# Performance work log

Measured on AMD Instinct MI355X. Metric: run time of the kernel, lower is better.

## Reference

```python
import jax, jax.numpy as jnp
import numpy as np

KS = 3
N = KS * KS
PAD = 1


def conv2d(x, w, b, stride=1, pad=0):
    out = jax.lax.conv_general_dilated(x, w, (stride, stride), [(pad, pad), (pad, pad)],
                                       dimension_numbers=('NCHW', 'OIHW', 'NCHW'))
    return out + b[None, :, None, None]


def lrelu(x):
    return jnp.where(x > 0, x, 0.2 * x)


# bicubic x2 upsample: half-pixel centers, cubic a=-0.75, replicate edges (matches torch F.interpolate bicubic)
_W_F75 = np.array([-0.03515625, 0.26171875, 0.87890625, -0.10546875], np.float32)  # frac 0.75 (even out idx)
_W_F25 = _W_F75[::-1].copy()  # frac 0.25 (odd out idx)


def _up2_axis(x, axis):
    n = x.shape[axis]
    j = np.arange(2 * n)
    c = (j + 0.5) / 2.0 - 0.5
    i0 = np.floor(c).astype(np.int32)
    taps = np.clip(i0[:, None] + np.arange(-1, 3)[None, :], 0, n - 1)  # [2n,4]
    w = np.where((j % 2 == 0)[:, None], _W_F75[None, :], _W_F25[None, :]).astype(np.float32)
    xm = jnp.moveaxis(x, axis, -1)
    g = xm[..., jnp.asarray(taps)]  # [..., 2n, 4]
    out = jnp.einsum('...jt,jt->...j', g, jnp.asarray(w))
    return jnp.moveaxis(out, -1, axis)


def bicubic_up2(x):
    return _up2_axis(_up2_axis(x, 2), 3)


def head(x, cw, cb, ra_w, ra_b, rb_w, rb_b):
    # Conv5x5 -> LReLU -> ResBlock -> LReLU
    h = lrelu(conv2d(x, cw, cb, pad=2))
    r = conv2d(lrelu(conv2d(h, ra_w, ra_b, pad=1)), rb_w, rb_b, pad=1) + h
    return lrelu(r)


def aligned_forward(x, query, ref, c1_w, c1_b, r1a_w, r1a_b, r1b_w, r1b_b,
                    p1_w, p1_b, r2a_w, r2a_b, r2b_w, r2b_b, p2_w, p2_b):
    q_up = bicubic_up2(query)
    rf = head(ref, c1_w, c1_b, r1a_w, r1a_b, r1b_w, r1b_b)
    qf = head(q_up, c1_w, c1_b, r1a_w, r1a_b, r1b_w, r1b_b)
    cat = jnp.concatenate([rf, qf], axis=1)
    h1 = lrelu(conv2d(cat, p1_w, p1_b, pad=2))
    h1 = lrelu(conv2d(lrelu(conv2d(h1, r2a_w, r2a_b, pad=1)), r2b_w, r2b_b, pad=1) + h1)
    aff = conv2d(h1, p2_w, p2_b, pad=0) + 1.0
    aff = jnp.clip(aff, -3.0, 3.0)
    b, _, h, w = aff.shape
    aff = jnp.transpose(aff, (0, 2, 3, 1))  # [b,h,w,3]
    s_x = aff[..., 0:1]
    s_y = aff[..., 1:2]
    theta = (aff[..., 2:3] - 1.0) * 1.0472
    vals = jnp.array([-1.5, -0.5, 0.5], aff.dtype)  # kernel offsets for ks=3
    pn_x = jnp.repeat(vals, KS)  # [N]
    pn_y = jnp.tile(vals, KS)
    px0 = pn_x * s_x  # [b,h,w,N] scaled kernel offsets
    py0 = pn_y * s_y
    ct = jnp.cos(theta)
    st = jnp.sin(theta)
    rx = px0 * ct - py0 * st  # rotate
    ry = px0 * st + py0 * ct
    px = rx + 1.5 + (jnp.arange(h, dtype=aff.dtype) + 1.0)[None, :, None, None]
    py = ry + 1.5 + (jnp.arange(w, dtype=aff.dtype) + 1.0)[None, None, :, None]
    xp = jnp.pad(x, ((0, 0), (0, 0), (PAD, PAD), (PAD, PAD)), mode='reflect')
    bsz, c, Hp, Wp = xp.shape
    fx = jnp.floor(px)
    fy = jnp.floor(py)
    qltx = jnp.clip(fx, 0, Hp - 1)
    qlty = jnp.clip(fy, 0, Wp - 1)
    qrbx = jnp.clip(fx + 1, 0, Hp - 1)
    qrby = jnp.clip(fy + 1, 0, Wp - 1)
    pxc = jnp.clip(px, 0, Hp - 1)
    pyc = jnp.clip(py, 0, Wp - 1)
    g_lt = (1 + (qltx - pxc)) * (1 + (qlty - pyc))
    g_rb = (1 - (qrbx - pxc)) * (1 - (qrby - pyc))
    g_lb = (1 + (qltx - pxc)) * (1 - (qrby - pyc))
    g_rt = (1 - (qrbx - pxc)) * (1 + (qlty - pyc))
    x_flat = xp.reshape(bsz, c, Hp * Wp)

    def gather(qx, qy):
        idx = (qx.astype(jnp.int32) * Wp + qy.astype(jnp.int32)).reshape(bsz, 1, -1)
        v = jnp.take_along_axis(x_flat, jnp.broadcast_to(idx, (bsz, c, idx.shape[-1])), axis=2)
        return v.reshape(bsz, c, h, w, N)

    align = (g_lt[:, None] * gather(qltx, qlty) + g_rb[:, None] * gather(qrbx, qrby)
             + g_lb[:, None] * gather(qltx, qrby) + g_rt[:, None] * gather(qrbx, qlty))
    # [b,c,h,w,N] -> [b,c,h*ks,w*ks]
    out = align.reshape(bsz, c, h, w, KS, KS).transpose(0, 1, 2, 4, 3, 5).reshape(bsz, c, h * KS, w * KS)
    return out


def setup_inputs() -> dict:
    key = jax.random.key(0)
    ks = jax.random.split(key, 10)

    def W(k, shape):
        fan_in = int(np.prod(shape[1:]))
        return jax.random.normal(k, shape, jnp.float32) / np.sqrt(fan_in)

    return {
        'x': jax.random.normal(ks[0], (2, 32, 256, 256), jnp.float32),
        'query': jax.random.normal(ks[1], (2, 3, 128, 128), jnp.float32),
        'ref': jax.random.normal(ks[2], (2, 3, 256, 256), jnp.float32),
        'c1_w': W(ks[3], (32, 3, 5, 5)), 'c1_b': jnp.zeros((32,), jnp.float32),
        'r1a_w': W(ks[4], (32, 32, 3, 3)), 'r1a_b': jnp.zeros((32,), jnp.float32),
        'r1b_w': W(ks[5], (32, 32, 3, 3)), 'r1b_b': jnp.zeros((32,), jnp.float32),
        'p1_w': W(ks[6], (32, 64, 5, 5)), 'p1_b': jnp.zeros((32,), jnp.float32),
        'r2a_w': W(ks[7], (32, 32, 3, 3)), 'r2a_b': jnp.zeros((32,), jnp.float32),
        'r2b_w': W(ks[8], (32, 32, 3, 3)), 'r2b_b': jnp.zeros((32,), jnp.float32),
        'p2_w': W(ks[9], (3, 32, 1, 1)), 'p2_b': jnp.zeros((3,), jnp.float32),
    }


def reference(x, query, ref, c1_w, c1_b, r1a_w, r1a_b, r1b_w, r1b_b,
              p1_w, p1_b, r2a_w, r2a_b, r2b_w, r2b_b, p2_w, p2_b):
    return aligned_forward(x, query, ref, c1_w, c1_b, r1a_w, r1a_b, r1b_w, r1b_b,
                           p1_w, p1_b, r2a_w, r2a_b, r2b_w, r2b_b, p2_w, p2_b)
```

## Files before the change

### kernel.cpp

```cpp
#include <hip/hip_runtime.h>
#include <math.h>

#define HW 65536

__device__ __forceinline__ float lrelu_f(float v) { return v > 0.f ? v : 0.2f * v; }

__global__ __launch_bounds__(256) void repack_all(
    const float* __restrict__ c1_w, float* __restrict__ wr_c1,
    const float* __restrict__ r1a_w, float* __restrict__ wr_r1a,
    const float* __restrict__ r1b_w, float* __restrict__ wr_r1b,
    const float* __restrict__ p1_w, float* __restrict__ wr_p1,
    const float* __restrict__ r2a_w, float* __restrict__ wr_r2a,
    const float* __restrict__ r2b_w, float* __restrict__ wr_r2b) {
  int i = blockIdx.x * 256 + threadIdx.x;
  const float* src;
  float* dst;
  int IC, KK, base;
  if (i < 2400)        { src = c1_w;  dst = wr_c1;  IC = 3;  KK = 25; base = 0; }
  else if (i < 11616)  { src = r1a_w; dst = wr_r1a; IC = 32; KK = 9;  base = 2400; }
  else if (i < 20832)  { src = r1b_w; dst = wr_r1b; IC = 32; KK = 9;  base = 11616; }
  else if (i < 72032)  { src = p1_w;  dst = wr_p1;  IC = 64; KK = 25; base = 20832; }
  else if (i < 81248)  { src = r2a_w; dst = wr_r2a; IC = 32; KK = 9;  base = 72032; }
  else if (i < 90464)  { src = r2b_w; dst = wr_r2b; IC = 32; KK = 9;  base = 81248; }
  else return;
  int j = i - base;
  int ickk = IC * KK;
  int o = j / ickk;
  int r = j - o * ickk;
  int ic = r / KK;
  int k = r - ic * KK;
  dst[((ic * 4 + (o >> 3)) * KK + k) * 8 + (o & 7)] = src[j];
}

__global__ __launch_bounds__(256) void up2_kernel(const float* __restrict__ q,
                                                  float* __restrict__ out) {
  int gid = blockIdx.x * blockDim.x + threadIdx.x;
  if (gid >= 2 * 3 * HW) return;
  int x = gid & 255;
  int y = (gid >> 8) & 255;
  int pc = gid >> 16;
  const float F[4] = {-0.03515625f, 0.26171875f, 0.87890625f, -0.10546875f};
  int iy[4], ix[4];
  float wy[4], wx[4];
  {
    int k = y >> 1; bool even = !(y & 1); int i0 = even ? k - 1 : k;
#pragma unroll
    for (int t = 0; t < 4; ++t) {
      int ii = i0 - 1 + t;
      iy[t] = min(max(ii, 0), 127);
      wy[t] = even ? F[t] : F[3 - t];
    }
  }
  {
    int k = x >> 1; bool even = !(x & 1); int i0 = even ? k - 1 : k;
#pragma unroll
    for (int t = 0; t < 4; ++t) {
      int ii = i0 - 1 + t;
      ix[t] = min(max(ii, 0), 127);
      wx[t] = even ? F[t] : F[3 - t];
    }
  }
  const float* qp = q + pc * 16384;
  float s = 0.f;
#pragma unroll
  for (int i = 0; i < 4; ++i) {
    float rs = 0.f;
#pragma unroll
    for (int j = 0; j < 4; ++j) rs = fmaf(wx[j], qp[iy[i] * 128 + ix[j]], rs);
    s = fmaf(wy[i], rs, s);
  }
  out[gid] = s;
}


__global__ __launch_bounds__(256) void conv5_c1(const float* __restrict__ in,
                                                const float* __restrict__ wr,
                                                const float* __restrict__ bias,
                                                float* __restrict__ out) {
  __shared__ float sm[3][8][24];
  int blk = blockIdx.x;
  int b = blk >> 10;
  int t = blk & 1023;
  int ty0 = (t >> 4) * 4, tx0 = (t & 15) * 16;
  int tid = threadIdx.x;
  for (int i = tid; i < 3 * 160; i += 256) {
    int ic = i / 160;
    int r2 = i - ic * 160;
    int r = r2 / 20;
    int c = r2 - r * 20;
    int gy = ty0 + r - 2, gx = tx0 + c - 2;
    float v = 0.f;
    if ((unsigned)gy < 256u && (unsigned)gx < 256u) v = in[(b * 3 + ic) * HW + gy * 256 + gx];
    sm[ic][r][c] = v;
  }
  __syncthreads();
  int lane = tid & 63;
  int wv = __builtin_amdgcn_readfirstlane(tid >> 6);
  int py = lane >> 4, px = lane & 15;
  float acc[8];
#pragma unroll
  for (int o = 0; o < 8; ++o) acc[o] = bias[wv * 8 + o];
#pragma unroll
  for (int ic = 0; ic < 3; ++ic) {
    const float* wp = wr + (ic * 4 + wv) * 200;
#pragma unroll
    for (int ky = 0; ky < 5; ++ky)
#pragma unroll
      for (int kx = 0; kx < 5; ++kx) {
        float v = sm[ic][py + ky][px + kx];
        const float* w8 = wp + (ky * 5 + kx) * 8;
#pragma unroll
        for (int o = 0; o < 8; ++o) acc[o] = fmaf(v, w8[o], acc[o]);
      }
  }
  int y = ty0 + py, x = tx0 + px;
#pragma unroll
  for (int o = 0; o < 8; ++o)
    out[(b * 32 + wv * 8 + o) * HW + y * 256 + x] = lrelu_f(acc[o]);
}

template <bool RES>
__global__ __launch_bounds__(256) void conv3_32(const float* __restrict__ in, int in_cs,
                                                const float* __restrict__ wr,
                                                const float* __restrict__ bias,
                                                const float* __restrict__ res,
                                                float* __restrict__ out, int out_cs,
                                                int out_co) {
  __shared__ float sm[32][6][24];
  int blk = blockIdx.x;
  int b = blk >> 10;
  int t = blk & 1023;
  int ty0 = (t >> 4) * 4, tx0 = (t & 15) * 16;
  int tid = threadIdx.x;
  for (int i = tid; i < 32 * 108; i += 256) {
    int ic = i / 108;
    int r2 = i - ic * 108;
    int r = r2 / 18;
    int c = r2 - r * 18;
    int gy = ty0 + r - 1, gx = tx0 + c - 1;
    float v = 0.f;
    if ((unsigned)gy < 256u && (unsigned)gx < 256u)
      v = in[(b * in_cs + ic) * HW + gy * 256 + gx];
    sm[ic][r][c] = v;
  }
  __syncthreads();
  int lane = tid & 63;
  int wv = __builtin_amdgcn_readfirstlane(tid >> 6);
  int py = lane >> 4, px = lane & 15;
  float acc[8];
#pragma unroll
  for (int o = 0; o < 8; ++o) acc[o] = bias[wv * 8 + o];
#pragma unroll 4
  for (int ic = 0; ic < 32; ++ic) {
    const float* wp = wr + (ic * 4 + wv) * 72;
#pragma unroll
    for (int ky = 0; ky < 3; ++ky)
#pragma unroll
      for (int kx = 0; kx < 3; ++kx) {
        float v = sm[ic][py + ky][px + kx];
        const float* w8 = wp + (ky * 3 + kx) * 8;
#pragma unroll
        for (int o = 0; o < 8; ++o) acc[o] = fmaf(v, w8[o], acc[o]);
      }
  }
  int y = ty0 + py, x = tx0 + px;
  int co = out_co + wv * 8;
#pragma unroll
  for (int o = 0; o < 8; ++o) {
    float rv = acc[o];
    if (RES) rv += res[(b * 32 + wv * 8 + o) * HW + y * 256 + x];
    out[(b * out_cs + co + o) * HW + y * 256 + x] = lrelu_f(rv);
  }
}

__global__ __launch_bounds__(256) void conv5_p1(const float* __restrict__ in,
                                                const float* __restrict__ wr,
                                                const float* __restrict__ bias,
                                                float* __restrict__ out) {
  __shared__ float sm[32][8][24];
  int blk = blockIdx.x;
  int b = blk >> 10;
  int t = blk & 1023;
  int ty0 = (t >> 4) * 4, tx0 = (t & 15) * 16;
  int tid = threadIdx.x;
  int lane = tid & 63;
  int wv = __builtin_amdgcn_readfirstlane(tid >> 6);
  int py = lane >> 4, px = lane & 15;
  float acc[8];
#pragma unroll
  for (int o = 0; o < 8; ++o) acc[o] = bias[wv * 8 + o];
#pragma unroll
  for (int ch = 0; ch < 2; ++ch) {
    __syncthreads();
    for (int i = tid; i < 32 * 160; i += 256) {
      int ic = i / 160;
      int r2 = i - ic * 160;
      int r = r2 / 20;
      int c = r2 - r * 20;
      int gy = ty0 + r - 2, gx = tx0 + c - 2;
      float v = 0.f;
      if ((unsigned)gy < 256u && (unsigned)gx < 256u)
        v = in[(b * 64 + ch * 32 + ic) * HW + gy * 256 + gx];
      sm[ic][r][c] = v;
    }
    __syncthreads();
#pragma unroll 2
    for (int ic = 0; ic < 32; ++ic) {
      const float* wp = wr + ((ch * 32 + ic) * 4 + wv) * 200;
#pragma unroll
      for (int ky = 0; ky < 5; ++ky)
#pragma unroll
        for (int kx = 0; kx < 5; ++kx) {
          float v = sm[ic][py + ky][px + kx];
          const float* w8 = wp + (ky * 5 + kx) * 8;
#pragma unroll
          for (int o = 0; o < 8; ++o) acc[o] = fmaf(v, w8[o], acc[o]);
        }
    }
  }
  int y = ty0 + py, x = tx0 + px;
#pragma unroll
  for (int o = 0; o < 8; ++o)
    out[(b * 32 + wv * 8 + o) * HW + y * 256 + x] = lrelu_f(acc[o]);
}

__global__ __launch_bounds__(256) void p2_aff(const float* __restrict__ h2,
                                              const float* __restrict__ w,
                                              const float* __restrict__ bias,
                                              float4* __restrict__ par) {
  int gid = blockIdx.x * 256 + threadIdx.x;
  int b = gid >> 16;
  int p = gid & 65535;
  float a0 = bias[0], a1 = bias[1], a2 = bias[2];
  for (int c = 0; c < 32; ++c) {
    float v = h2[(b * 32 + c) * HW + p];
    a0 = fmaf(v, w[c], a0);
    a1 = fmaf(v, w[32 + c], a1);
    a2 = fmaf(v, w[64 + c], a2);
  }
  a0 = fminf(fmaxf(a0 + 1.f, -3.f), 3.f);
  a1 = fminf(fmaxf(a1 + 1.f, -3.f), 3.f);
  a2 = fminf(fmaxf(a2 + 1.f, -3.f), 3.f);
  float th = (a2 - 1.f) * 1.0472f;
  float4 o;
  o.x = a0;
  o.y = a1;
  o.z = cosf(th);
  o.w = sinf(th);
  par[gid] = o;
}

__device__ __forceinline__ int refl_idx(int k) {
  int s = k - 1;
  s = s < 0 ? -s : s;
  s = s > 255 ? 510 - s : s;
  return s;
}

__global__ __launch_bounds__(256) void sample_kernel(const float* __restrict__ x,
                                                     const float4* __restrict__ par,
                                                     float* __restrict__ out) {
  const int total = 2 * 32 * 768 * 768;
  int stride = gridDim.x * 256;
  for (int gid = blockIdx.x * 256 + threadIdx.x; gid < total; gid += stride) {
    int ox = gid % 768;
    int t1 = gid / 768;
    int oy = t1 % 768;
    int t2 = t1 / 768;
    int c = t2 & 31;
    int b = t2 >> 5;
    int xw = ox / 3;
    int kj = ox - 3 * xw;
    int y = oy / 3;
    int ki = oy - 3 * y;
    float4 pr = par[(b << 16) + y * 256 + xw];
    float px0 = ((float)ki - 1.5f) * pr.x;
    float py0 = ((float)kj - 1.5f) * pr.y;
    float ct = pr.z, st = pr.w;
    float px = px0 * ct - py0 * st + 1.5f + (float)(y + 1);
    float py = px0 * st + py0 * ct + 1.5f + (float)(xw + 1);
    float fx = floorf(px), fy = floorf(py);
    float x0f = fminf(fmaxf(fx, 0.f), 257.f);
    float x1f = fminf(fmaxf(fx + 1.f, 0.f), 257.f);
    float y0f = fminf(fmaxf(fy, 0.f), 257.f);
    float y1f = fminf(fmaxf(fy + 1.f, 0.f), 257.f);
    float pxc = fminf(fmaxf(px, 0.f), 257.f);
    float pyc = fminf(fmaxf(py, 0.f), 257.f);
    float dx0 = 1.f + (x0f - pxc), dx1 = 1.f - (x1f - pxc);
    float dy0 = 1.f + (y0f - pyc), dy1 = 1.f - (y1f - pyc);
    int xi0 = refl_idx((int)x0f), xi1 = refl_idx((int)x1f);
    int yi0 = refl_idx((int)y0f), yi1 = refl_idx((int)y1f);
    const float* xp = x + (size_t)(b * 32 + c) * HW;
    float v = dx0 * dy0 * xp[xi0 * 256 + yi0] + dx1 * dy1 * xp[xi1 * 256 + yi1] +
              dx0 * dy1 * xp[xi0 * 256 + yi1] + dx1 * dy0 * xp[xi1 * 256 + yi0];
    out[gid] = v;
  }
}

extern "C" void kernel_launch(void* const* d_in, const int* in_sizes, int n_in,
                              void* d_out, int out_size, void* d_ws, size_t ws_size,
                              hipStream_t stream) {
  const float* x = (const float*)d_in[0];
  const float* query = (const float*)d_in[1];
  const float* ref = (const float*)d_in[2];
  const float* c1_w = (const float*)d_in[3];
  const float* c1_b = (const float*)d_in[4];
  const float* r1a_w = (const float*)d_in[5];
  const float* r1a_b = (const float*)d_in[6];
  const float* r1b_w = (const float*)d_in[7];
  const float* r1b_b = (const float*)d_in[8];
  const float* p1_w = (const float*)d_in[9];
  const float* p1_b = (const float*)d_in[10];
  const float* r2a_w = (const float*)d_in[11];
  const float* r2a_b = (const float*)d_in[12];
  const float* r2b_w = (const float*)d_in[13];
  const float* r2b_b = (const float*)d_in[14];
  const float* p2_w = (const float*)d_in[15];
  const float* p2_b = (const float*)d_in[16];
  float* out = (float*)d_out;

  float* ws = (float*)d_ws;
  float* qup = ws;
  float* cat = qup + 393216;
  float* t1 = cat + 8388608;
  float* t2 = t1 + 4194304;
  float* h1 = t2 + 4194304;
  float4* par = (float4*)(h1 + 4194304);
  float* wr_c1 = (float*)(par + 131072);
  float* wr_r1a = wr_c1 + 2400;
  float* wr_r1b = wr_r1a + 9216;
  float* wr_p1 = wr_r1b + 9216;
  float* wr_r2a = wr_p1 + 51200;
  float* wr_r2b = wr_r2a + 9216;

  repack_all<<<354, 256, 0, stream>>>(c1_w, wr_c1, r1a_w, wr_r1a, r1b_w, wr_r1b,
                                      p1_w, wr_p1, r2a_w, wr_r2a, r2b_w, wr_r2b);

  up2_kernel<<<1536, 256, 0, stream>>>(query, qup);

  conv5_c1<<<2048, 256, 0, stream>>>(ref, wr_c1, c1_b, t1);
  conv3_32<false><<<2048, 256, 0, stream>>>(t1, 32, wr_r1a, r1a_b, nullptr, t2, 32, 0);
  conv3_32<true><<<2048, 256, 0, stream>>>(t2, 32, wr_r1b, r1b_b, t1, cat, 64, 0);

  conv5_c1<<<2048, 256, 0, stream>>>(qup, wr_c1, c1_b, t1);
  conv3_32<false><<<2048, 256, 0, stream>>>(t1, 32, wr_r1a, r1a_b, nullptr, t2, 32, 0);
  conv3_32<true><<<2048, 256, 0, stream>>>(t2, 32, wr_r1b, r1b_b, t1, cat, 64, 32);

  conv5_p1<<<2048, 256, 0, stream>>>(cat, wr_p1, p1_b, h1);
  conv3_32<false><<<2048, 256, 0, stream>>>(h1, 32, wr_r2a, r2a_b, nullptr, t2, 32, 0);
  conv3_32<true><<<2048, 256, 0, stream>>>(t2, 32, wr_r2b, r2b_b, h1, t1, 32, 0);

  p2_aff<<<512, 256, 0, stream>>>(t1, p2_w, p2_b, par);

  sample_kernel<<<4096, 256, 0, stream>>>(x, par, out);
}
```

Before: 765.4 us.

## Retile convs by output-channel group and hoist sampling coords across channels

The conv kernels now tile 8x32 pixels per block, with one 8-output-channel group per block selected by the block index, and stream input channels through shared memory in chunks of 8. Previously each 4x16 block covered all 32 output channels. This gives every wave the same weights (uniform/scalar loads) and enlarges the spatial tile, cutting halo overhead, but input tiles are now reloaded once per output-channel group. The sampling kernel computes the 9 bilinear offsets and weights once per pixel and reuses them across 8 channels, removing repeated index math. The cost is register pressure and strided, less coalesced output stores (stride 3).

```diff
diff --git a/kernel.cpp b/kernel.cpp
--- a/kernel.cpp
+++ b/kernel.cpp
@@ -77,17 +77,18 @@
                                                 const float* __restrict__ wr,
                                                 const float* __restrict__ bias,
                                                 float* __restrict__ out) {
-  __shared__ float sm[3][8][24];
+  __shared__ float sm[3][12][36];
   int blk = blockIdx.x;
   int b = blk >> 10;
-  int t = blk & 1023;
-  int ty0 = (t >> 4) * 4, tx0 = (t & 15) * 16;
+  int ocg = (blk >> 8) & 3;
+  int tile = blk & 255;
+  int ty0 = (tile >> 3) * 8, tx0 = (tile & 7) * 32;
   int tid = threadIdx.x;
-  for (int i = tid; i < 3 * 160; i += 256) {
-    int ic = i / 160;
-    int r2 = i - ic * 160;
-    int r = r2 / 20;
-    int c = r2 - r * 20;
+  for (int i = tid; i < 3 * 432; i += 256) {
+    int ic = i / 432;
+    int rem = i - ic * 432;
+    int r = rem / 36;
+    int c = rem - r * 36;
     int gy = ty0 + r - 2, gx = tx0 + c - 2;
     float v = 0.f;
     if ((unsigned)gy < 256u && (unsigned)gx < 256u) v = in[(b * 3 + ic) * HW + gy * 256 + gx];
@@ -96,13 +97,13 @@
   __syncthreads();
   int lane = tid & 63;
   int wv = __builtin_amdgcn_readfirstlane(tid >> 6);
-  int py = lane >> 4, px = lane & 15;
+  int py = 2 * wv + (lane >> 5), px = lane & 31;
   float acc[8];
 #pragma unroll
-  for (int o = 0; o < 8; ++o) acc[o] = bias[wv * 8 + o];
+  for (int o = 0; o < 8; ++o) acc[o] = bias[ocg * 8 + o];
 #pragma unroll
   for (int ic = 0; ic < 3; ++ic) {
-    const float* wp = wr + (ic * 4 + wv) * 200;
+    const float* wp = wr + (ic * 4 + ocg) * 200;
 #pragma unroll
     for (int ky = 0; ky < 5; ++ky)
 #pragma unroll
@@ -116,7 +117,7 @@
   int y = ty0 + py, x = tx0 + px;
 #pragma unroll
   for (int o = 0; o < 8; ++o)
-    out[(b * 32 + wv * 8 + o) * HW + y * 256 + x] = lrelu_f(acc[o]);
+    out[(b * 32 + ocg * 8 + o) * HW + y * 256 + x] = lrelu_f(acc[o]);
 }
 
 template <bool RES>
@@ -126,49 +127,54 @@
                                                 const float* __restrict__ res,
                                                 float* __restrict__ out, int out_cs,
                                                 int out_co) {
-  __shared__ float sm[32][6][24];
+  __shared__ float sm[8][10][34];
   int blk = blockIdx.x;
   int b = blk >> 10;
-  int t = blk & 1023;
-  int ty0 = (t >> 4) * 4, tx0 = (t & 15) * 16;
+  int ocg = (blk >> 8) & 3;
+  int tile = blk & 255;
+  int ty0 = (tile >> 3) * 8, tx0 = (tile & 7) * 32;
   int tid = threadIdx.x;
-  for (int i = tid; i < 32 * 108; i += 256) {
-    int ic = i / 108;
-    int r2 = i - ic * 108;
-    int r = r2 / 18;
-    int c = r2 - r * 18;
-    int gy = ty0 + r - 1, gx = tx0 + c - 1;
-    float v = 0.f;
-    if ((unsigned)gy < 256u && (unsigned)gx < 256u)
-      v = in[(b * in_cs + ic) * HW + gy * 256 + gx];
-    sm[ic][r][c] = v;
-  }
-  __syncthreads();
   int lane = tid & 63;
   int wv = __builtin_amdgcn_readfirstlane(tid >> 6);
-  int py = lane >> 4, px = lane & 15;
+  int py = 2 * wv + (lane >> 5), px = lane & 31;
   float acc[8];
 #pragma unroll
-  for (int o = 0; o < 8; ++o) acc[o] = bias[wv * 8 + o];
-#pragma unroll 4
-  for (int ic = 0; ic < 32; ++ic) {
-    const float* wp = wr + (ic * 4 + wv) * 72;
-#pragma unroll
-    for (int ky = 0; ky < 3; ++ky)
-#pragma unroll
-      for (int kx = 0; kx < 3; ++kx) {
-        float v = sm[ic][py + ky][px + kx];
-        const float* w8 = wp + (ky * 3 + kx) * 8;
-#pragma unroll
-        for (int o = 0; o < 8; ++o) acc[o] = fmaf(v, w8[o], acc[o]);
-      }
+  for (int o = 0; o < 8; ++o) acc[o] = bias[ocg * 8 + o];
+#pragma unroll 1
+  for (int ch = 0; ch < 4; ++ch) {
+    __syncthreads();
+    for (int i = tid; i < 8 * 340; i += 256) {
+      int ic = i / 340;
+      int rem = i - ic * 340;
+      int r = rem / 34;
+      int c = rem - r * 34;
+      int gy = ty0 + r - 1, gx = tx0 + c - 1;
+      float v = 0.f;
+      if ((unsigned)gy < 256u && (unsigned)gx < 256u)
+        v = in[(b * in_cs + ch * 8 + ic) * HW + gy * 256 + gx];
+      sm[ic][r][c] = v;
+    }
+    __syncthreads();
+#pragma unroll 2
+    for (int ic = 0; ic < 8; ++ic) {
+      const float* wp = wr + ((ch * 8 + ic) * 4 + ocg) * 72;
+#pragma unroll
+      for (int ky = 0; ky < 3; ++ky)
+#pragma unroll
+        for (int kx = 0; kx < 3; ++kx) {
+          float v = sm[ic][py + ky][px + kx];
+          const float* w8 = wp + (ky * 3 + kx) * 8;
+#pragma unroll
+          for (int o = 0; o < 8; ++o) acc[o] = fmaf(v, w8[o], acc[o]);
+        }
+    }
   }
   int y = ty0 + py, x = tx0 + px;
-  int co = out_co + wv * 8;
+  int co = out_co + ocg * 8;
 #pragma unroll
   for (int o = 0; o < 8; ++o) {
     float rv = acc[o];
-    if (RES) rv += res[(b * 32 + wv * 8 + o) * HW + y * 256 + x];
+    if (RES) rv += res[(b * 32 + ocg * 8 + o) * HW + y * 256 + x];
     out[(b * out_cs + co + o) * HW + y * 256 + x] = lrelu_f(rv);
   }
 }
@@ -177,36 +183,37 @@
                                                 const float* __restrict__ wr,
                                                 const float* __restrict__ bias,
                                                 float* __restrict__ out) {
-  __shared__ float sm[32][8][24];
+  __shared__ float sm[8][12][36];
   int blk = blockIdx.x;
   int b = blk >> 10;
-  int t = blk & 1023;
-  int ty0 = (t >> 4) * 4, tx0 = (t & 15) * 16;
+  int ocg = (blk >> 8) & 3;
+  int tile = blk & 255;
+  int ty0 = (tile >> 3) * 8, tx0 = (tile & 7) * 32;
   int tid = threadIdx.x;
   int lane = tid & 63;
   int wv = __builtin_amdgcn_readfirstlane(tid >> 6);
-  int py = lane >> 4, px = lane & 15;
+  int py = 2 * wv + (lane >> 5), px = lane & 31;
   float acc[8];
 #pragma unroll
-  for (int o = 0; o < 8; ++o) acc[o] = bias[wv * 8 + o];
-#pragma unroll
-  for (int ch = 0; ch < 2; ++ch) {
+  for (int o = 0; o < 8; ++o) acc[o] = bias[ocg * 8 + o];
+#pragma unroll 1
+  for (int ch = 0; ch < 8; ++ch) {
     __syncthreads();
-    for (int i = tid; i < 32 * 160; i += 256) {
-      int ic = i / 160;
-      int r2 = i - ic * 160;
-      int r = r2 / 20;
-      int c = r2 - r * 20;
+    for (int i = tid; i < 8 * 432; i += 256) {
+      int ic = i / 432;
+      int rem = i - ic * 432;
+      int r = rem / 36;
+      int c = rem - r * 36;
       int gy = ty0 + r - 2, gx = tx0 + c - 2;
       float v = 0.f;
       if ((unsigned)gy < 256u && (unsigned)gx < 256u)
-        v = in[(b * 64 + ch * 32 + ic) * HW + gy * 256 + gx];
+        v = in[(b * 64 + ch * 8 + ic) * HW + gy * 256 + gx];
       sm[ic][r][c] = v;
     }
     __syncthreads();
 #pragma unroll 2
-    for (int ic = 0; ic < 32; ++ic) {
-      const float* wp = wr + ((ch * 32 + ic) * 4 + wv) * 200;
+    for (int ic = 0; ic < 8; ++ic) {
+      const float* wp = wr + ((ch * 8 + ic) * 4 + ocg) * 200;
 #pragma unroll
       for (int ky = 0; ky < 5; ++ky)
 #pragma unroll
@@ -221,7 +228,7 @@
   int y = ty0 + py, x = tx0 + px;
 #pragma unroll
   for (int o = 0; o < 8; ++o)
-    out[(b * 32 + wv * 8 + o) * HW + y * 256 + x] = lrelu_f(acc[o]);
+    out[(b * 32 + ocg * 8 + o) * HW + y * 256 + x] = lrelu_f(acc[o]);
 }
 
 __global__ __launch_bounds__(256) void p2_aff(const float* __restrict__ h2,
@@ -260,40 +267,59 @@
 __global__ __launch_bounds__(256) void sample_kernel(const float* __restrict__ x,
                                                      const float4* __restrict__ par,
                                                      float* __restrict__ out) {
-  const int total = 2 * 32 * 768 * 768;
-  int stride = gridDim.x * 256;
-  for (int gid = blockIdx.x * 256 + threadIdx.x; gid < total; gid += stride) {
-    int ox = gid % 768;
-    int t1 = gid / 768;
-    int oy = t1 % 768;
-    int t2 = t1 / 768;
-    int c = t2 & 31;
-    int b = t2 >> 5;
-    int xw = ox / 3;
-    int kj = ox - 3 * xw;
-    int y = oy / 3;
-    int ki = oy - 3 * y;
-    float4 pr = par[(b << 16) + y * 256 + xw];
-    float px0 = ((float)ki - 1.5f) * pr.x;
-    float py0 = ((float)kj - 1.5f) * pr.y;
-    float ct = pr.z, st = pr.w;
-    float px = px0 * ct - py0 * st + 1.5f + (float)(y + 1);
-    float py = px0 * st + py0 * ct + 1.5f + (float)(xw + 1);
-    float fx = floorf(px), fy = floorf(py);
-    float x0f = fminf(fmaxf(fx, 0.f), 257.f);
-    float x1f = fminf(fmaxf(fx + 1.f, 0.f), 257.f);
-    float y0f = fminf(fmaxf(fy, 0.f), 257.f);
-    float y1f = fminf(fmaxf(fy + 1.f, 0.f), 257.f);
-    float pxc = fminf(fmaxf(px, 0.f), 257.f);
-    float pyc = fminf(fmaxf(py, 0.f), 257.f);
-    float dx0 = 1.f + (x0f - pxc), dx1 = 1.f - (x1f - pxc);
-    float dy0 = 1.f + (y0f - pyc), dy1 = 1.f - (y1f - pyc);
-    int xi0 = refl_idx((int)x0f), xi1 = refl_idx((int)x1f);
-    int yi0 = refl_idx((int)y0f), yi1 = refl_idx((int)y1f);
+  int gid = blockIdx.x * 256 + threadIdx.x;
+  int xw = gid & 255;
+  int y = (gid >> 8) & 255;
+  int cg = (gid >> 16) & 3;
+  int b = gid >> 18;
+  float4 pr = par[(b << 16) + y * 256 + xw];
+  float sx = pr.x, sy = pr.y, ct = pr.z, st = pr.w;
+  int off[9][4];
+  float g[9][4];
+#pragma unroll
+  for (int ki = 0; ki < 3; ++ki)
+#pragma unroll
+    for (int kj = 0; kj < 3; ++kj) {
+      int n = ki * 3 + kj;
+      float px0 = ((float)ki - 1.5f) * sx;
+      float py0 = ((float)kj - 1.5f) * sy;
+      float px = px0 * ct - py0 * st + 1.5f + (float)(y + 1);
+      float py = px0 * st + py0 * ct + 1.5f + (float)(xw + 1);
+      float fx = floorf(px), fy = floorf(py);
+      float x0f = fminf(fmaxf(fx, 0.f), 257.f);
+      float x1f = fminf(fmaxf(fx + 1.f, 0.f), 257.f);
+      float y0f = fminf(fmaxf(fy, 0.f), 257.f);
+      float y1f = fminf(fmaxf(fy + 1.f, 0.f), 257.f);
+      float pxc = fminf(fmaxf(px, 0.f), 257.f);
+      float pyc = fminf(fmaxf(py, 0.f), 257.f);
+      float dx0 = 1.f + (x0f - pxc), dx1 = 1.f - (x1f - pxc);
+      float dy0 = 1.f + (y0f - pyc), dy1 = 1.f - (y1f - pyc);
+      g[n][0] = dx0 * dy0;
+      g[n][1] = dx1 * dy1;
+      g[n][2] = dx0 * dy1;
+      g[n][3] = dx1 * dy0;
+      int xi0 = refl_idx((int)x0f), xi1 = refl_idx((int)x1f);
+      int yi0 = refl_idx((int)y0f), yi1 = refl_idx((int)y1f);
+      off[n][0] = xi0 * 256 + yi0;
+      off[n][1] = xi1 * 256 + yi1;
+      off[n][2] = xi0 * 256 + yi1;
+      off[n][3] = xi1 * 256 + yi0;
+    }
+#pragma unroll 1
+  for (int cc = 0; cc < 8; ++cc) {
+    int c = cg * 8 + cc;
     const float* xp = x + (size_t)(b * 32 + c) * HW;
-    float v = dx0 * dy0 * xp[xi0 * 256 + yi0] + dx1 * dy1 * xp[xi1 * 256 + yi1] +
-              dx0 * dy1 * xp[xi0 * 256 + yi1] + dx1 * dy0 * xp[xi1 * 256 + yi0];
-    out[gid] = v;
+    float* op = out + ((size_t)(b * 32 + c) * 768 + 3 * y) * 768 + 3 * xw;
+#pragma unroll
+    for (int ki = 0; ki < 3; ++ki) {
+#pragma unroll
+      for (int kj = 0; kj < 3; ++kj) {
+        int n = ki * 3 + kj;
+        float v = g[n][0] * xp[off[n][0]] + g[n][1] * xp[off[n][1]] +
+                  g[n][2] * xp[off[n][2]] + g[n][3] * xp[off[n][3]];
+        op[ki * 768 + kj] = v;
+      }
+    }
   }
 }
 
@@ -352,5 +378,5 @@
 
   p2_aff<<<512, 256, 0, stream>>>(t1, p2_w, p2_b, par);
 
-  sample_kernel<<<4096, 256, 0, stream>>>(x, par, out);
-}
+  sample_kernel<<<2048, 256, 0, stream>>>(x, par, out);
+}
```

New measurement: 884.7 us. +15.6%, slower.
